# Kernel optimization log

Measured on AMD Instinct MI355X. Metric: run time of the kernel, lower is better.

Reference implementation:

```python
import jax, jax.numpy as jnp
import numpy as np

PATCH = 8
EPS = 1e-5


def setup_inputs() -> dict:
    key = jax.random.key(0)
    k0, k1, k2 = jax.random.split(key, 3)
    B, C, H, W = 8, 256, 256, 256
    r = 8
    x = jax.random.normal(k0, (B, C, H, W), dtype=jnp.float32)
    gamma = jnp.ones((C,), dtype=jnp.float32)   # LayerNorm weight
    beta = jnp.zeros((C,), dtype=jnp.float32)   # LayerNorm bias
    # torch Linear weights: [out, in], bias=False
    w1 = jax.random.normal(k1, (C // r, C), dtype=jnp.float32) * (1.0 / np.sqrt(C))
    w2 = jax.random.normal(k2, (C, C // r), dtype=jnp.float32) * (1.0 / np.sqrt(C // r))
    return {"x": x, "gamma": gamma, "beta": beta, "w1": w1, "w2": w2}


def reference(x, gamma, beta, w1, w2):
    # x: [B, C, H, W]; H, W divisible by PATCH (no-pad path of the module)
    B, C, H, W = x.shape
    ph = pw = PATCH
    nH, nW = H // ph, W // pw

    # LayerNorm over channel dim (module permutes patches to channel-last before norm;
    # per-pixel channel LN is invariant to the patch regrouping)
    xcl = jnp.transpose(x, (0, 2, 3, 1))                    # [B, H, W, C]
    mu = jnp.mean(xcl, axis=-1, keepdims=True)
    var = jnp.mean(jnp.square(xcl - mu), axis=-1, keepdims=True)
    xn = (xcl - mu) * jax.lax.rsqrt(var + EPS) * gamma + beta

    # patchify: [B, nH, ph, nW, pw, C]
    xp = xn.reshape(B, nH, ph, nW, pw, C)

    # per-patch, per-channel mean of the normalized tensor -> [B, nH, nW, C]
    pm = jnp.mean(xp, axis=(2, 4))

    # SE-style gating MLP (Linear no bias -> SiLU -> Linear no bias -> sigmoid)
    h = jax.nn.silu(jnp.einsum('bijc,rc->bijr', pm, w1))    # [B, nH, nW, C//r]
    gate = jax.nn.sigmoid(jnp.einsum('bijr,cr->bijc', h, w2))  # [B, nH, nW, C]

    # scale normalized patches by per-patch channel gates and scatter back
    out = xp * gate[:, :, None, :, None, :]                 # [B, nH, ph, nW, pw, C]
    out = out.reshape(B, H, W, C)
    return jnp.transpose(out, (0, 3, 1, 2))                 # [B, C, H, W]
```

## Files before the change

### kernel.cpp

```cpp
#include <hip/hip_runtime.h>
#include <math.h>

#define C_DIM 256
#define HWDIM 256
#define CH_STRIDE (HWDIM * HWDIM)
#define R_DIM 32

__global__ __launch_bounds__(1024, 4)
void lpa_fused_kernel(const float* __restrict__ x,
                      const float* __restrict__ gamma,
                      const float* __restrict__ beta,
                      const float* __restrict__ w1,
                      const float* __restrict__ w2,
                      float* __restrict__ out)
{
    __shared__ float sp[16 * 256];
    __shared__ float sq[16 * 256];
    __shared__ float mu_s[256];
    __shared__ float rs_s[256];
    __shared__ float gs[C_DIM];
    __shared__ float bs[C_DIM];
    __shared__ float pm_s[4 * C_DIM];
    __shared__ float h_s[4 * R_DIM];
    __shared__ float A_s[4 * C_DIM];
    __shared__ float B_s[4 * C_DIM];

    const int t    = threadIdx.x;
    const int wid  = t >> 6;
    const int lane = t & 63;
    const int hh   = lane >> 3;
    const int wq   = lane & 7;
    const int pat  = wq >> 1;

    const int bid = blockIdx.x;
    const int b   = bid >> 8;
    const int ij  = bid & 255;
    const unsigned H0 = (unsigned)(ij >> 3) * 8u;
    const unsigned W0 = (unsigned)(ij & 7) * 32u;
    const unsigned baseb  = (unsigned)b * (C_DIM * CH_STRIDE);
    const unsigned rowoff = baseb + (H0 + hh) * HWDIM + W0 + (unsigned)wq * 4u;

    if (t < C_DIM) { gs[t] = gamma[t]; bs[t] = beta[t]; }

    const float* xb = x + rowoff + (unsigned)wid * 16u * CH_STRIDE;

    float4 v[16];
    float s0 = 0.f, s1 = 0.f, s2 = 0.f, s3 = 0.f;
    float q0 = 0.f, q1 = 0.f, q2 = 0.f, q3 = 0.f;
#pragma unroll
    for (int k = 0; k < 16; ++k) {
        v[k] = *reinterpret_cast<const float4*>(xb + (unsigned)k * CH_STRIDE);
        s0 += v[k].x; q0 += v[k].x * v[k].x;
        s1 += v[k].y; q1 += v[k].y * v[k].y;
        s2 += v[k].z; q2 += v[k].z * v[k].z;
        s3 += v[k].w; q3 += v[k].w * v[k].w;
    }
    const int p0 = hh * 32 + wq * 4;
    *reinterpret_cast<float4*>(&sp[wid * 256 + p0]) = make_float4(s0, s1, s2, s3);
    *reinterpret_cast<float4*>(&sq[wid * 256 + p0]) = make_float4(q0, q1, q2, q3);
    __syncthreads();

    if (t < 256) {
        float s = 0.f, q = 0.f;
#pragma unroll
        for (int w = 0; w < 16; ++w) {
            s += sp[w * 256 + t];
            q += sq[w * 256 + t];
        }
        float mu  = s * (1.0f / 256.0f);
        float var = q * (1.0f / 256.0f) - mu * mu;
        mu_s[t] = mu;
        rs_s[t] = rsqrtf(var + 1e-5f);
    }
    __syncthreads();

    const float mu0 = mu_s[p0 + 0], mu1 = mu_s[p0 + 1];
    const float mu2 = mu_s[p0 + 2], mu3 = mu_s[p0 + 3];
    const float r0 = rs_s[p0 + 0], r1 = rs_s[p0 + 1];
    const float r2 = rs_s[p0 + 2], r3 = rs_s[p0 + 3];
#pragma unroll
    for (int k = 0; k < 16; ++k) {
        int c = wid * 16 + k;
        float wsum = r0 * (v[k].x - mu0) + r1 * (v[k].y - mu1)
                   + r2 * (v[k].z - mu2) + r3 * (v[k].w - mu3);
        wsum += __shfl_xor(wsum, 1);
        wsum += __shfl_xor(wsum, 8);
        wsum += __shfl_xor(wsum, 16);
        wsum += __shfl_xor(wsum, 32);
        if ((lane & 57) == 0) {
            pm_s[pat * C_DIM + c] = gs[c] * wsum * (1.0f / 64.0f) + bs[c];
        }
    }
    __syncthreads();

    {
        const int pat4 = t >> 8;
        const int r    = (t >> 3) & 31;
        const int k8   = t & 7;
        const float4* wrow = reinterpret_cast<const float4*>(w1 + r * C_DIM + k8 * 32);
        const float* pmk = &pm_s[pat4 * C_DIM + k8 * 32];
        float s = 0.f;
#pragma unroll
        for (int j = 0; j < 8; ++j) {
            float4 wv = wrow[j];
            float4 pv = *reinterpret_cast<const float4*>(pmk + j * 4);
            s += wv.x * pv.x + wv.y * pv.y + wv.z * pv.z + wv.w * pv.w;
        }
        s += __shfl_down(s, 4, 8);
        s += __shfl_down(s, 2, 8);
        s += __shfl_down(s, 1, 8);
        if (k8 == 0) {
            float sig = 1.0f / (1.0f + __expf(-s));
            h_s[pat4 * R_DIM + r] = s * sig;
        }
    }
    __syncthreads();

    {
        const int pat4 = t >> 8;
        const int c4   = t & 255;
        const float4* wrow = reinterpret_cast<const float4*>(w2 + c4 * R_DIM);
        const float* hk = &h_s[pat4 * R_DIM];
        float s = 0.f;
#pragma unroll
        for (int j = 0; j < 8; ++j) {
            float4 wv = wrow[j];
            s += wv.x * hk[j * 4 + 0] + wv.y * hk[j * 4 + 1]
               + wv.z * hk[j * 4 + 2] + wv.w * hk[j * 4 + 3];
        }
        float gate = 1.0f / (1.0f + __expf(-s));
        A_s[pat4 * C_DIM + c4] = gs[c4] * gate;
        B_s[pat4 * C_DIM + c4] = bs[c4] * gate;
    }
    __syncthreads();

    float* ob = out + rowoff + (unsigned)wid * 16u * CH_STRIDE;
#pragma unroll
    for (int k = 0; k < 16; ++k) {
        int c = wid * 16 + k;
        float a  = A_s[pat * C_DIM + c];
        float bb = B_s[pat * C_DIM + c];
        float4 o;
        o.x = a * r0 * (v[k].x - mu0) + bb;
        o.y = a * r1 * (v[k].y - mu1) + bb;
        o.z = a * r2 * (v[k].z - mu2) + bb;
        o.w = a * r3 * (v[k].w - mu3) + bb;
        *reinterpret_cast<float4*>(ob + (unsigned)k * CH_STRIDE) = o;
    }
}

extern "C" void kernel_launch(void* const* d_in, const int* in_sizes, int n_in,
                              void* d_out, int out_size, void* d_ws, size_t ws_size,
                              hipStream_t stream) {
    const float* x     = (const float*)d_in[0];
    const float* gamma = (const float*)d_in[1];
    const float* beta  = (const float*)d_in[2];
    const float* w1    = (const float*)d_in[3];
    const float* w2    = (const float*)d_in[4];
    float* out = (float*)d_out;

    const int B = in_sizes[0] / (C_DIM * HWDIM * HWDIM);
    const int nwg = B * 256;

    lpa_fused_kernel<<<nwg, 1024, 0, stream>>>(x, gamma, beta, w1, w2, out);
}
```

Baseline: 258.5 us.

## Halve block tile to 8x16 pixels, remap XCD blocks, replace shuffles with LDS reduction

Each block now covers an 8x16 pixel tile (two patches) with 512 threads instead of 8x32 with 1024. Each wave handles two channel groups with 64-byte row segments. Blocks are remapped so that consecutive work IDs land on the same XCD. The per-patch channel mean drops the cross-lane shuffle reduction in favour of a padded LDS partial-sum buffer followed by a column reduction. The aim is finer scheduling granularity and less shuffle work, at the cost of shorter contiguous memory segments and an extra LDS pass and barrier.

```diff
diff --git a/kernel.cpp b/kernel.cpp
--- a/kernel.cpp
+++ b/kernel.cpp
@@ -5,67 +5,75 @@
 #define HWDIM 256
 #define CH_STRIDE (HWDIM * HWDIM)
 #define R_DIM 32
+#define PS_PITCH 257
 
-__global__ __launch_bounds__(1024, 4)
+__global__ __launch_bounds__(512, 4)
 void lpa_fused_kernel(const float* __restrict__ x,
                       const float* __restrict__ gamma,
                       const float* __restrict__ beta,
                       const float* __restrict__ w1,
                       const float* __restrict__ w2,
-                      float* __restrict__ out)
+                      float* __restrict__ out,
+                      int nwg)
 {
-    __shared__ float sp[16 * 256];
-    __shared__ float sq[16 * 256];
-    __shared__ float mu_s[256];
-    __shared__ float rs_s[256];
+    __shared__ float sp[16 * 128];
+    __shared__ float sq[16 * 128];
+    __shared__ float ps[32 * PS_PITCH];
+    __shared__ float mu_s[128];
+    __shared__ float rs_s[128];
     __shared__ float gs[C_DIM];
     __shared__ float bs[C_DIM];
-    __shared__ float pm_s[4 * C_DIM];
-    __shared__ float h_s[4 * R_DIM];
-    __shared__ float A_s[4 * C_DIM];
-    __shared__ float B_s[4 * C_DIM];
+    __shared__ float pm_s[2 * C_DIM];
+    __shared__ float h_s[2 * R_DIM];
+    __shared__ float2 AB_s[2 * C_DIM];
 
     const int t    = threadIdx.x;
     const int wid  = t >> 6;
     const int lane = t & 63;
-    const int hh   = lane >> 3;
-    const int wq   = lane & 7;
-    const int pat  = wq >> 1;
+    const int co     = lane >> 5;
+    const int rowpos = (lane >> 2) & 7;
+    const int f4c    = lane & 3;
+    const int patch  = f4c >> 1;
+    const int p0     = rowpos * 16 + f4c * 4;
 
     const int bid = blockIdx.x;
-    const int b   = bid >> 8;
-    const int ij  = bid & 255;
-    const unsigned H0 = (unsigned)(ij >> 3) * 8u;
-    const unsigned W0 = (unsigned)(ij & 7) * 32u;
+    const int per_xcd = nwg >> 3;
+    const int pid = (bid & 7) * per_xcd + (bid >> 3);
+
+    const int b  = pid >> 9;
+    const int ij = pid & 511;
+    const unsigned H0 = (unsigned)(ij >> 4) * 8u;
+    const unsigned W0 = (unsigned)(ij & 15) * 16u;
     const unsigned baseb  = (unsigned)b * (C_DIM * CH_STRIDE);
-    const unsigned rowoff = baseb + (H0 + hh) * HWDIM + W0 + (unsigned)wq * 4u;
+    const unsigned rowoff = baseb + (H0 + rowpos) * HWDIM + W0 + (unsigned)f4c * 4u;
+    const unsigned c0 = (unsigned)wid * 32u + (unsigned)co;
 
     if (t < C_DIM) { gs[t] = gamma[t]; bs[t] = beta[t]; }
 
-    const float* xb = x + rowoff + (unsigned)wid * 16u * CH_STRIDE;
+    const float* xb = x + rowoff + c0 * CH_STRIDE;
 
     float4 v[16];
     float s0 = 0.f, s1 = 0.f, s2 = 0.f, s3 = 0.f;
     float q0 = 0.f, q1 = 0.f, q2 = 0.f, q3 = 0.f;
 #pragma unroll
     for (int k = 0; k < 16; ++k) {
-        v[k] = *reinterpret_cast<const float4*>(xb + (unsigned)k * CH_STRIDE);
+        v[k] = *reinterpret_cast<const float4*>(xb + (unsigned)(2 * k) * CH_STRIDE);
         s0 += v[k].x; q0 += v[k].x * v[k].x;
         s1 += v[k].y; q1 += v[k].y * v[k].y;
         s2 += v[k].z; q2 += v[k].z * v[k].z;
         s3 += v[k].w; q3 += v[k].w * v[k].w;
     }
-    const int p0 = hh * 32 + wq * 4;
-    *reinterpret_cast<float4*>(&sp[wid * 256 + p0]) = make_float4(s0, s1, s2, s3);
-    *reinterpret_cast<float4*>(&sq[wid * 256 + p0]) = make_float4(q0, q1, q2, q3);
+    const int grp = wid * 2 + co;
+    *reinterpret_cast<float4*>(&sp[grp * 128 + p0]) = make_float4(s0, s1, s2, s3);
+    *reinterpret_cast<float4*>(&sq[grp * 128 + p0]) = make_float4(q0, q1, q2, q3);
     __syncthreads();
 
-    if (t < 256) {
+    if (t < 128) {
         float s = 0.f, q = 0.f;
 #pragma unroll
-        for (int w = 0; w < 16; ++w) {
-            s += sp[w * 256 + t];
-            q += sq[w * 256 + t];
+        for (int g = 0; g < 16; ++g) {
+            s += sp[g * 128 + t];
+            q += sq[g * 128 + t];
         }
         float mu  = s * (1.0f / 256.0f);
         float var = q * (1.0f / 256.0f) - mu * mu;
@@ -74,31 +82,36 @@
     }
     __syncthreads();
 
-    const float mu0 = mu_s[p0 + 0], mu1 = mu_s[p0 + 1];
-    const float mu2 = mu_s[p0 + 2], mu3 = mu_s[p0 + 3];
-    const float r0 = rs_s[p0 + 0], r1 = rs_s[p0 + 1];
-    const float r2 = rs_s[p0 + 2], r3 = rs_s[p0 + 3];
+    const float4 mu4 = *reinterpret_cast<const float4*>(&mu_s[p0]);
+    const float4 rs4 = *reinterpret_cast<const float4*>(&rs_s[p0]);
+    const int slot = patch * 16 + (f4c & 1) + rowpos * 2;
 #pragma unroll
     for (int k = 0; k < 16; ++k) {
-        int c = wid * 16 + k;
-        float wsum = r0 * (v[k].x - mu0) + r1 * (v[k].y - mu1)
-                   + r2 * (v[k].z - mu2) + r3 * (v[k].w - mu3);
-        wsum += __shfl_xor(wsum, 1);
-        wsum += __shfl_xor(wsum, 8);
-        wsum += __shfl_xor(wsum, 16);
-        wsum += __shfl_xor(wsum, 32);
-        if ((lane & 57) == 0) {
-            pm_s[pat * C_DIM + c] = gs[c] * wsum * (1.0f / 64.0f) + bs[c];
-        }
+        unsigned c = c0 + (unsigned)(2 * k);
+        float wsum = rs4.x * (v[k].x - mu4.x) + rs4.y * (v[k].y - mu4.y)
+                   + rs4.z * (v[k].z - mu4.z) + rs4.w * (v[k].w - mu4.w);
+        ps[slot * PS_PITCH + c] = wsum;
     }
     __syncthreads();
 
     {
-        const int pat4 = t >> 8;
-        const int r    = (t >> 3) & 31;
-        const int k8   = t & 7;
+        const int pt = t >> 8;
+        const int c  = t & 255;
+        float s = 0.f;
+#pragma unroll
+        for (int sub = 0; sub < 16; ++sub) {
+            s += ps[(pt * 16 + sub) * PS_PITCH + c];
+        }
+        pm_s[pt * C_DIM + c] = gs[c] * s * (1.0f / 64.0f) + bs[c];
+    }
+    __syncthreads();
+
+    {
+        const int pt = t >> 8;
+        const int r  = (t >> 3) & 31;
+        const int k8 = t & 7;
         const float4* wrow = reinterpret_cast<const float4*>(w1 + r * C_DIM + k8 * 32);
-        const float* pmk = &pm_s[pat4 * C_DIM + k8 * 32];
+        const float* pmk = &pm_s[pt * C_DIM + k8 * 32];
         float s = 0.f;
 #pragma unroll
         for (int j = 0; j < 8; ++j) {
@@ -111,16 +124,16 @@
         s += __shfl_down(s, 1, 8);
         if (k8 == 0) {
             float sig = 1.0f / (1.0f + __expf(-s));
-            h_s[pat4 * R_DIM + r] = s * sig;
+            h_s[pt * R_DIM + r] = s * sig;
         }
     }
     __syncthreads();
 
     {
-        const int pat4 = t >> 8;
-        const int c4   = t & 255;
-        const float4* wrow = reinterpret_cast<const float4*>(w2 + c4 * R_DIM);
-        const float* hk = &h_s[pat4 * R_DIM];
+        const int pt = t >> 8;
+        const int c  = t & 255;
+        const float4* wrow = reinterpret_cast<const float4*>(w2 + c * R_DIM);
+        const float* hk = &h_s[pt * R_DIM];
         float s = 0.f;
 #pragma unroll
         for (int j = 0; j < 8; ++j) {
@@ -129,23 +142,21 @@
                + wv.z * hk[j * 4 + 2] + wv.w * hk[j * 4 + 3];
         }
         float gate = 1.0f / (1.0f + __expf(-s));
-        A_s[pat4 * C_DIM + c4] = gs[c4] * gate;
-        B_s[pat4 * C_DIM + c4] = bs[c4] * gate;
+        AB_s[pt * C_DIM + c] = make_float2(gs[c] * gate, bs[c] * gate);
     }
     __syncthreads();
 
-    float* ob = out + rowoff + (unsigned)wid * 16u * CH_STRIDE;
+    float* ob = out + rowoff + c0 * CH_STRIDE;
 #pragma unroll
     for (int k = 0; k < 16; ++k) {
-        int c = wid * 16 + k;
-        float a  = A_s[pat * C_DIM + c];
-        float bb = B_s[pat * C_DIM + c];
+        unsigned c = c0 + (unsigned)(2 * k);
+        float2 ab = AB_s[patch * C_DIM + c];
         float4 o;
-        o.x = a * r0 * (v[k].x - mu0) + bb;
-        o.y = a * r1 * (v[k].y - mu1) + bb;
-        o.z = a * r2 * (v[k].z - mu2) + bb;
-        o.w = a * r3 * (v[k].w - mu3) + bb;
-        *reinterpret_cast<float4*>(ob + (unsigned)k * CH_STRIDE) = o;
+        o.x = ab.x * rs4.x * (v[k].x - mu4.x) + ab.y;
+        o.y = ab.x * rs4.y * (v[k].y - mu4.y) + ab.y;
+        o.z = ab.x * rs4.z * (v[k].z - mu4.z) + ab.y;
+        o.w = ab.x * rs4.w * (v[k].w - mu4.w) + ab.y;
+        *reinterpret_cast<float4*>(ob + (unsigned)(2 * k) * CH_STRIDE) = o;
     }
 }
 
@@ -160,7 +171,7 @@
     float* out = (float*)d_out;
 
     const int B = in_sizes[0] / (C_DIM * HWDIM * HWDIM);
-    const int nwg = B * 256;
+    const int nwg = B * 512;
 
-    lpa_fused_kernel<<<nwg, 1024, 0, stream>>>(x, gamma, beta, w1, w2, out);
+    lpa_fused_kernel<<<nwg, 512, 0, stream>>>(x, gamma, beta, w1, w2, out, nwg);
 }
```

Measured after the change: 289.4 us. +11.9%, slower.

## Replace shuffle patch-mean reduction with LDS transpose, nontemporal stores

Applied to the files above, without the earlier changes.

Replaces the per-channel warp-shuffle reduction for patch means with per-lane partial sums written to a padded LDS buffer, then a per-thread row sum. Packs the A/B gate scales into a float2, vectorizes the mu/rstd loads, and uses nontemporal stores for the output. Launch bounds drop to 2 blocks, and the extra 65 KB LDS buffer raises shared memory per block, which may limit occupancy of this memory-bound kernel.

```diff
diff --git a/kernel.cpp b/kernel.cpp
--- a/kernel.cpp
+++ b/kernel.cpp
@@ -5,8 +5,11 @@
 #define HWDIM 256
 #define CH_STRIDE (HWDIM * HWDIM)
 #define R_DIM 32
+#define PS_PITCH 65
 
-__global__ __launch_bounds__(1024, 4)
+typedef float nfloat4 __attribute__((ext_vector_type(4)));
+
+__global__ __launch_bounds__(1024, 2)
 void lpa_fused_kernel(const float* __restrict__ x,
                       const float* __restrict__ gamma,
                       const float* __restrict__ beta,
@@ -16,14 +19,14 @@
 {
     __shared__ float sp[16 * 256];
     __shared__ float sq[16 * 256];
+    __shared__ float ps[C_DIM * PS_PITCH];
     __shared__ float mu_s[256];
     __shared__ float rs_s[256];
     __shared__ float gs[C_DIM];
     __shared__ float bs[C_DIM];
     __shared__ float pm_s[4 * C_DIM];
     __shared__ float h_s[4 * R_DIM];
-    __shared__ float A_s[4 * C_DIM];
-    __shared__ float B_s[4 * C_DIM];
+    __shared__ float2 AB_s[4 * C_DIM];
 
     const int t    = threadIdx.x;
     const int wid  = t >> 6;
@@ -31,6 +34,8 @@
     const int hh   = lane >> 3;
     const int wq   = lane & 7;
     const int pat  = wq >> 1;
+    const int p0   = hh * 32 + wq * 4;
+    const int slot = pat * 16 + hh * 2 + (wq & 1);
 
     const int bid = blockIdx.x;
     const int b   = bid >> 8;
@@ -55,7 +60,6 @@
         s2 += v[k].z; q2 += v[k].z * v[k].z;
         s3 += v[k].w; q3 += v[k].w * v[k].w;
     }
-    const int p0 = hh * 32 + wq * 4;
     *reinterpret_cast<float4*>(&sp[wid * 256 + p0]) = make_float4(s0, s1, s2, s3);
     *reinterpret_cast<float4*>(&sq[wid * 256 + p0]) = make_float4(q0, q1, q2, q3);
     __syncthreads();
@@ -74,22 +78,26 @@
     }
     __syncthreads();
 
-    const float mu0 = mu_s[p0 + 0], mu1 = mu_s[p0 + 1];
-    const float mu2 = mu_s[p0 + 2], mu3 = mu_s[p0 + 3];
-    const float r0 = rs_s[p0 + 0], r1 = rs_s[p0 + 1];
-    const float r2 = rs_s[p0 + 2], r3 = rs_s[p0 + 3];
+    const float4 mu4 = *reinterpret_cast<const float4*>(&mu_s[p0]);
+    const float4 rs4 = *reinterpret_cast<const float4*>(&rs_s[p0]);
+
 #pragma unroll
     for (int k = 0; k < 16; ++k) {
         int c = wid * 16 + k;
-        float wsum = r0 * (v[k].x - mu0) + r1 * (v[k].y - mu1)
-                   + r2 * (v[k].z - mu2) + r3 * (v[k].w - mu3);
-        wsum += __shfl_xor(wsum, 1);
-        wsum += __shfl_xor(wsum, 8);
-        wsum += __shfl_xor(wsum, 16);
-        wsum += __shfl_xor(wsum, 32);
-        if ((lane & 57) == 0) {
-            pm_s[pat * C_DIM + c] = gs[c] * wsum * (1.0f / 64.0f) + bs[c];
-        }
+        float wsum = rs4.x * (v[k].x - mu4.x) + rs4.y * (v[k].y - mu4.y)
+                   + rs4.z * (v[k].z - mu4.z) + rs4.w * (v[k].w - mu4.w);
+        ps[c * PS_PITCH + slot] = wsum;
+    }
+    __syncthreads();
+
+    {
+        const int pt = t >> 8;
+        const int c  = t & 255;
+        const float* row = &ps[c * PS_PITCH + pt * 16];
+        float s = 0.f;
+#pragma unroll
+        for (int j = 0; j < 16; ++j) s += row[j];
+        pm_s[pt * C_DIM + c] = gs[c] * s * (1.0f / 64.0f) + bs[c];
     }
     __syncthreads();
 
@@ -129,23 +137,24 @@
                + wv.z * hk[j * 4 + 2] + wv.w * hk[j * 4 + 3];
         }
         float gate = 1.0f / (1.0f + __expf(-s));
-        A_s[pat4 * C_DIM + c4] = gs[c4] * gate;
-        B_s[pat4 * C_DIM + c4] = bs[c4] * gate;
+        AB_s[pat4 * C_DIM + c4] = make_float2(gs[c4] * gate, bs[c4] * gate);
     }
     __syncthreads();
 
-    float* ob = out + rowoff + (unsigned)wid * 16u * CH_STRIDE;
+    {
+        float* ob = out + rowoff + (unsigned)wid * 16u * CH_STRIDE;
 #pragma unroll
-    for (int k = 0; k < 16; ++k) {
-        int c = wid * 16 + k;
-        float a  = A_s[pat * C_DIM + c];
-        float bb = B_s[pat * C_DIM + c];
-        float4 o;
-        o.x = a * r0 * (v[k].x - mu0) + bb;
-        o.y = a * r1 * (v[k].y - mu1) + bb;
-        o.z = a * r2 * (v[k].z - mu2) + bb;
-        o.w = a * r3 * (v[k].w - mu3) + bb;
-        *reinterpret_cast<float4*>(ob + (unsigned)k * CH_STRIDE) = o;
+        for (int k = 0; k < 16; ++k) {
+            int c = wid * 16 + k;
+            float2 ab = AB_s[pat * C_DIM + c];
+            nfloat4 o;
+            o.x = ab.x * rs4.x * (v[k].x - mu4.x) + ab.y;
+            o.y = ab.x * rs4.y * (v[k].y - mu4.y) + ab.y;
+            o.z = ab.x * rs4.z * (v[k].z - mu4.z) + ab.y;
+            o.w = ab.x * rs4.w * (v[k].w - mu4.w) + ab.y;
+            __builtin_nontemporal_store(o,
+                reinterpret_cast<nfloat4*>(ob + (unsigned)k * CH_STRIDE));
+        }
     }
 }
 
```

Result: faster. 247.3 us (-4.4%).
